# Kernel optimization log

Measured on AMD Instinct MI355X. Metric: run time of the kernel, lower is better.

## Reference

```python
import jax, jax.numpy as jnp
import numpy as np

N, M = 30000, 16
NFEAT, NCLASS = 1024, 16
K, DD = 8, 32          # ncaps, nhidden (delta_d)
D = K * DD             # rep_dim = 256
NLAYER = 3


def _l2norm(x, axis):
    n = jnp.linalg.norm(x, axis=axis, keepdims=True)
    return x / jnp.maximum(n, 1e-12)


def _routing(x, neighbors, max_iter, param, fc_w=None, fc_b=None):
    # x: [n, d]; neighbors: [n, m] int indices in [0, n] (n = zero pad row)
    n = x.shape[0]
    m = neighbors.shape[1]
    if fc_w is not None:  # first layer: per-capsule linear + relu
        x_dis = _l2norm(x.reshape(n, K, DD), axis=2)
        # torch Linear: y = x @ W.T + b, per capsule k
        x = jax.nn.relu(jnp.einsum('nki,koi->nko', x_dis, fc_w) + fc_b)
        x = x.reshape(n, D)
    x = _l2norm(x.reshape(n, K, DD), axis=2).reshape(n, D)
    z_tab = jnp.concatenate([x, jnp.zeros((1, D), x.dtype)], axis=0)
    z = z_tab[neighbors].reshape(n, m, K, DD)  # [n,m,k,dd] neighbor gather
    u_before = x.reshape(n, K, DD)
    u = None
    p1 = None
    for it in range(max_iter):
        if u is None:
            p = jnp.zeros((n, m, K), x.dtype)
        else:
            p = jnp.einsum('nmkd,nkd->nmk', z, u)
        p1 = jax.nn.softmax(p, axis=1)  # over neighbors
        u1 = jnp.einsum('nmkd,nmk->nkd', z, p1)
        p2 = jax.nn.softmax(p, axis=2)  # over capsules
        u2 = jnp.einsum('nmkd,nmk->nkd', z, p2)
        u = param * u1 + (1.0 - param) * u2 + u_before
        u_before = u
        if it < max_iter - 1:
            u = _l2norm(u, axis=2)
    return u.reshape(n, D), p1


def setup_inputs() -> dict:
    key = jax.random.key(0)
    ks = jax.random.split(key, 8)
    s = 1.0 / np.sqrt(D)
    return {
        'x': jax.random.normal(ks[0], (N, NFEAT), jnp.float32),
        'neighbors': jax.random.randint(ks[1], (N, M), 0, N).astype(jnp.int32),
        'pca_w': jax.random.normal(ks[2], (NFEAT, D), jnp.float32) * s,
        'pca_b': jax.random.normal(ks[3], (D,), jnp.float32) * s,
        'raw_param': jnp.ones((1,), jnp.float32),
        'fc_w': jax.random.normal(ks[4], (K, DD, DD), jnp.float32) * (1.0 / np.sqrt(DD)),
        'fc_b': jax.random.normal(ks[5], (K, DD), jnp.float32) * 0.01,
        'mlp_w': jax.random.normal(ks[6], (NCLASS, D), jnp.float32) * s,
        'mlp_b': jax.random.normal(ks[7], (NCLASS,), jnp.float32) * s,
        'routit': 6,
    }


def reference(x, neighbors, pca_w, pca_b, raw_param, fc_w, fc_b, mlp_w, mlp_b, routit):
    # pca projection (eval mode: dropout is identity)
    h = jax.nn.relu(x @ pca_w + pca_b)
    param = jax.nn.sigmoid(raw_param[0])
    for i in range(NLAYER - 1):
        h, _ = _routing(h, neighbors, routit, param,
                        fc_w if i == 0 else None, fc_b if i == 0 else None)
        h = jax.nn.relu(h)
    h, _ = _routing(h, neighbors, routit, param,
                    fc_w if NLAYER == 1 else None, fc_b if NLAYER == 1 else None)
    logit = h @ mlp_w.T + mlp_b
    log_probs = jax.nn.log_softmax(logit, axis=1)
    return log_probs, h  # (classifier output, embedding)
```

## Files before the change

### kernel.cpp

```cpp
#include <hip/hip_runtime.h>

#define NN 30000
#define MMN 16
#define NF 1024
#define NC 16
#define KC 8
#define DDIM 32
#define DR 256

typedef __bf16 bf16x8 __attribute__((ext_vector_type(8)));
typedef __bf16 bf16x4 __attribute__((ext_vector_type(4)));
typedef float floatx4 __attribute__((ext_vector_type(4)));

__device__ inline void splitbf(float v, __bf16& h, __bf16& l) {
  h = (__bf16)v;
  l = (__bf16)(v - (float)h);
}

template <int C>
__device__ __forceinline__ float dppadd(float x) {
  return x + __int_as_float(
      __builtin_amdgcn_update_dpp(0, __float_as_int(x), C, 0xF, 0xF, true));
}
template <int C>
__device__ __forceinline__ float dppmov(float x) {
  return __int_as_float(
      __builtin_amdgcn_update_dpp(0, __float_as_int(x), C, 0xF, 0xF, true));
}
__device__ __forceinline__ float red8(float x) {
  x = dppadd<0xB1>(x);
  x = dppadd<0x4E>(x);
  x = dppadd<0x141>(x);
  return x;
}
__device__ __forceinline__ float redk(float x) {
  x = dppadd<0x128>(x);
  x = x + __int_as_float(__builtin_amdgcn_ds_swizzle(__float_as_int(x), 0x401F));
  x = x + __shfl_xor(x, 32);
  return x;
}
__device__ __forceinline__ float red16sum(float x) {
  x = dppadd<0xB1>(x);
  x = dppadd<0x4E>(x);
  x = x + __int_as_float(__builtin_amdgcn_ds_swizzle(__float_as_int(x), 0x101F));
  x = x + __int_as_float(__builtin_amdgcn_ds_swizzle(__float_as_int(x), 0x201F));
  return x;
}
__device__ __forceinline__ float red16max(float x) {
  x = fmaxf(x, dppmov<0xB1>(x));
  x = fmaxf(x, dppmov<0x4E>(x));
  x = fmaxf(x, __int_as_float(__builtin_amdgcn_ds_swizzle(__float_as_int(x), 0x101F)));
  x = fmaxf(x, __int_as_float(__builtin_amdgcn_ds_swizzle(__float_as_int(x), 0x201F)));
  return x;
}

__device__ __forceinline__ float rscatter8(const float p[8], int lane) {
  const bool j4 = (lane & 4) != 0, j2 = (lane & 2) != 0, j1 = (lane & 1) != 0;
  float k0 = j4 ? p[4] : p[0];
  float k1 = j4 ? p[5] : p[1];
  float k2 = j4 ? p[6] : p[2];
  float k3 = j4 ? p[7] : p[3];
  float s0 = j4 ? p[0] : p[4];
  float s1 = j4 ? p[1] : p[5];
  float s2 = j4 ? p[2] : p[6];
  float s3 = j4 ? p[3] : p[7];
  k0 += dppmov<0x141>(s0); k1 += dppmov<0x141>(s1);
  k2 += dppmov<0x141>(s2); k3 += dppmov<0x141>(s3);
  float t0 = j2 ? k2 : k0;
  float t1 = j2 ? k3 : k1;
  float u0 = j2 ? k0 : k2;
  float u1 = j2 ? k1 : k3;
  t0 += dppmov<0x4E>(u0); t1 += dppmov<0x4E>(u1);
  float a = j1 ? t1 : t0;
  float b = j1 ? t0 : t1;
  a += dppmov<0xB1>(b);
  return a;
}

__device__ __forceinline__ void agather8(float a, float w[8], int lane) {
  const bool j4 = (lane & 4) != 0, j2 = (lane & 2) != 0, j1 = (lane & 1) != 0;
  float pa = dppmov<0xB1>(a);
  float b0 = j1 ? pa : a;
  float b1 = j1 ? a : pa;
  float p0 = dppmov<0x4E>(b0), p1 = dppmov<0x4E>(b1);
  float q0 = j2 ? p0 : b0;
  float q1 = j2 ? p1 : b1;
  float q2 = j2 ? b0 : p0;
  float q3 = j2 ? b1 : p1;
  float m0 = dppmov<0x141>(q0), m1 = dppmov<0x141>(q1);
  float m2 = dppmov<0x141>(q2), m3 = dppmov<0x141>(q3);
  w[0] = j4 ? m0 : q0;  w[1] = j4 ? m1 : q1;
  w[2] = j4 ? m2 : q2;  w[3] = j4 ? m3 : q3;
  w[4] = j4 ? q0 : m0;  w[5] = j4 ? q1 : m1;
  w[6] = j4 ? q2 : m2;  w[7] = j4 ? q3 : m3;
}

__global__ __launch_bounds__(256) void wt_build_kernel(
    const float* __restrict__ w, __bf16* __restrict__ wt_hi, __bf16* __restrict__ wt_lo) {
  const int gid  = blockIdx.x * 256 + threadIdx.x;
  const int lane = gid & 63;
  const int kc   = gid >> 10;
  const int g    = (gid >> 6) & 15;
  const int c = g * 16 + (lane & 15);
  const int k = kc * 32 + (lane >> 4) * 8;
  bf16x8 h, l;
#pragma unroll
  for (int j = 0; j < 8; ++j) {
    const float v = w[(size_t)(k + j) * DR + c];
    __bf16 hh, ll; splitbf(v, hh, ll);
    h[j] = hh; l[j] = ll;
  }
  *(bf16x8*)(wt_hi + (size_t)gid * 8) = h;
  *(bf16x8*)(wt_lo + (size_t)gid * 8) = l;
}

__global__ void pad_zero_kernel(float* __restrict__ p) {
  ((float4*)p)[threadIdx.x] = make_float4(0.f, 0.f, 0.f, 0.f);
}

__global__ __launch_bounds__(256, 4) void pca_mfma_kernel(
    const float* __restrict__ x, const __bf16* __restrict__ wt_hi,
    const __bf16* __restrict__ wt_lo, const float* __restrict__ b,
    float* __restrict__ out) {
  __shared__ __bf16 Ah[128][40];
  __shared__ __bf16 Al[128][40];
  const int t    = threadIdx.x;
  const int lane = t & 63;
  const int wv   = t >> 6;
  const int q    = lane >> 4;
  const int lm   = lane & 15;
  const int rowBase = (blockIdx.x >> 2) << 7;
  const int cg      = (blockIdx.x & 3) << 2;
  const int colBase = cg << 4;

  const int sr = t >> 2;
  const int sc = (t & 3) << 2;

  floatx4 acc[2][4];
#pragma unroll
  for (int rt = 0; rt < 2; ++rt)
#pragma unroll
    for (int ct = 0; ct < 4; ++ct)
      acc[rt][ct] = (floatx4){0.f, 0.f, 0.f, 0.f};

  const float* xrA = x + (size_t)(rowBase + sr) * NF + sc;
  const float* xrB = x + (size_t)(rowBase + sr + 64) * NF + sc;
  const bool okA = (rowBase + sr) < NN;
  const bool okB = (rowBase + sr + 64) < NN;

  const __bf16* wfh = wt_hi + ((size_t)cg << 9) + (lane << 3);
  const __bf16* wfl = wt_lo + ((size_t)cg << 9) + (lane << 3);

  float4 xv[4];
  xv[0] = okA ? *(const float4*)(xrA)      : make_float4(0.f, 0.f, 0.f, 0.f);
  xv[1] = okA ? *(const float4*)(xrA + 16) : make_float4(0.f, 0.f, 0.f, 0.f);
  xv[2] = okB ? *(const float4*)(xrB)      : make_float4(0.f, 0.f, 0.f, 0.f);
  xv[3] = okB ? *(const float4*)(xrB + 16) : make_float4(0.f, 0.f, 0.f, 0.f);

  for (int k0 = 0; k0 < NF; k0 += 32) {
    const int kc = k0 >> 5;
    bf16x8 bh[4], bl[4];
#pragma unroll
    for (int ct = 0; ct < 4; ++ct) {
      bh[ct] = *(const bf16x8*)(wfh + (((size_t)kc << 4) + ct) * 512);
      bl[ct] = *(const bf16x8*)(wfl + (((size_t)kc << 4) + ct) * 512);
    }
    asm volatile("s_waitcnt lgkmcnt(0)" ::: "memory");
    __builtin_amdgcn_s_barrier();
    {
#pragma unroll
      for (int i = 0; i < 4; ++i) {
        bf16x4 h4, l4;
        const float vs[4] = {xv[i].x, xv[i].y, xv[i].z, xv[i].w};
#pragma unroll
        for (int j = 0; j < 4; ++j) { __bf16 H, L; splitbf(vs[j], H, L); h4[j] = H; l4[j] = L; }
        const int row = sr + (i >> 1) * 64;
        const int col = sc + (i & 1) * 16;
        *(bf16x4*)&Ah[row][col] = h4;
        *(bf16x4*)&Al[row][col] = l4;
      }
    }
    float4 xn[4];
    if (k0 + 32 < NF) {
      xn[0] = okA ? *(const float4*)(xrA + k0 + 32) : make_float4(0.f, 0.f, 0.f, 0.f);
      xn[1] = okA ? *(const float4*)(xrA + k0 + 48) : make_float4(0.f, 0.f, 0.f, 0.f);
      xn[2] = okB ? *(const float4*)(xrB + k0 + 32) : make_float4(0.f, 0.f, 0.f, 0.f);
      xn[3] = okB ? *(const float4*)(xrB + k0 + 48) : make_float4(0.f, 0.f, 0.f, 0.f);
    } else {
#pragma unroll
      for (int i = 0; i < 4; ++i) xn[i] = make_float4(0.f, 0.f, 0.f, 0.f);
    }
    asm volatile("s_waitcnt lgkmcnt(0)" ::: "memory");
    __builtin_amdgcn_s_barrier();
#pragma unroll
    for (int rt = 0; rt < 2; ++rt) {
      const int ar = (wv << 5) + (rt << 4) + lm;
      const bf16x8 ah = *(const bf16x8*)&Ah[ar][q << 3];
      const bf16x8 al = *(const bf16x8*)&Al[ar][q << 3];
#pragma unroll
      for (int ct = 0; ct < 4; ++ct) {
        acc[rt][ct] = __builtin_amdgcn_mfma_f32_16x16x32_bf16(ah, bh[ct], acc[rt][ct], 0, 0, 0);
        acc[rt][ct] = __builtin_amdgcn_mfma_f32_16x16x32_bf16(ah, bl[ct], acc[rt][ct], 0, 0, 0);
        acc[rt][ct] = __builtin_amdgcn_mfma_f32_16x16x32_bf16(al, bh[ct], acc[rt][ct], 0, 0, 0);
      }
    }
#pragma unroll
    for (int i = 0; i < 4; ++i) xv[i] = xn[i];
  }
#pragma unroll
  for (int rt = 0; rt < 2; ++rt) {
#pragma unroll
    for (int ct = 0; ct < 4; ++ct) {
      const int col = colBase + (ct << 4) + lm;
      const float bias = b[col];
#pragma unroll
      for (int r = 0; r < 4; ++r) {
        const int row = rowBase + (wv << 5) + (rt << 4) + (q << 2) + r;
        if (row < NN) out[(size_t)row * DR + col] = fmaxf(acc[rt][ct][r] + bias, 0.f);
      }
    }
  }
}

__global__ __launch_bounds__(256, 4) void norm_fc_kernel(
    const float* __restrict__ hin, const float* __restrict__ fcw,
    const float* __restrict__ fcb, float* __restrict__ q) {
  const int k = blockIdx.y;
  const int n = blockIdx.x * 256 + threadIdx.x;
  if (n > NN) return;
  float* qrow = q + (size_t)n * DR + k * DDIM;
  if (n == NN) {
#pragma unroll
    for (int i = 0; i < DDIM; i += 4)
      *(float4*)(qrow + i) = make_float4(0.f, 0.f, 0.f, 0.f);
    return;
  }
  const float* hrow = hin + (size_t)n * DR + k * DDIM;
  float v[DDIM];
  float ss = 0.f;
#pragma unroll
  for (int i = 0; i < DDIM; i += 4) {
    float4 tv = *(const float4*)(hrow + i);
    tv.x = fmaxf(tv.x, 0.f); tv.y = fmaxf(tv.y, 0.f);
    tv.z = fmaxf(tv.z, 0.f); tv.w = fmaxf(tv.w, 0.f);
    v[i] = tv.x; v[i+1] = tv.y; v[i+2] = tv.z; v[i+3] = tv.w;
    ss += tv.x*tv.x + tv.y*tv.y + tv.z*tv.z + tv.w*tv.w;
  }
  float inv = 1.f / fmaxf(sqrtf(ss), 1e-12f);
#pragma unroll
  for (int i = 0; i < DDIM; ++i) v[i] *= inv;
#pragma unroll
  for (int i = 0; i < DDIM; ++i) asm volatile("" : "+v"(v[i]));
  float y[DDIM];
  ss = 0.f;
  const float* wk = fcw + (size_t)k * DDIM * DDIM;
  const float* bk = fcb + k * DDIM;
#pragma unroll 4
  for (int o = 0; o < DDIM; ++o) {
    float a = bk[o];
#pragma unroll
    for (int i = 0; i < DDIM; i += 4) {
      const float4 wv = *(const float4*)(wk + o * DDIM + i);
      a += v[i]*wv.x + v[i+1]*wv.y + v[i+2]*wv.z + v[i+3]*wv.w;
    }
    a = fmaxf(a, 0.f);
    y[o] = a;
    ss += a * a;
  }
  inv = 1.f / fmaxf(sqrtf(ss), 1e-12f);
#pragma unroll
  for (int o = 0; o < DDIM; o += 4) {
    float4 tv;
    tv.x = y[o]*inv; tv.y = y[o+1]*inv; tv.z = y[o+2]*inv; tv.w = y[o+3]*inv;
    *(float4*)(qrow + o) = tv;
  }
}

__global__ __launch_bounds__(256, 4) void routing_kernel(
    const float* __restrict__ tab, const float* __restrict__ padrow,
    const int* __restrict__ nbr, const float* __restrict__ rawp,
    const int* __restrict__ ritp, float* __restrict__ uout, const int doNorm) {
  const int lane = threadIdx.x & 63;
  const int node = blockIdx.x * 4 + (threadIdx.x >> 6);
  const int off = (lane >> 3) * DDIM + (lane & 7) * 4;
  const float param = 1.f / (1.f + __expf(-rawp[0]));
  const float qparam = 1.f - param;
  const int iters = ritp[0];

  float4 z[MMN];
#pragma unroll
  for (int m = 0; m < MMN; ++m) {
    const int j = nbr[node * MMN + m];
    const float* zrow = (j == NN) ? padrow : (tab + (size_t)j * DR);
    z[m] = *(const float4*)(zrow + off);
  }
  float4 ub = *(const float4*)(tab + (size_t)node * DR + off);

  float4 S = make_float4(0.f, 0.f, 0.f, 0.f);
#pragma unroll
  for (int m = 0; m < MMN; ++m) {
    S.x += z[m].x; S.y += z[m].y; S.z += z[m].z; S.w += z[m].w;
  }
  const float w0 = param * 0.0625f + qparam * 0.125f;
  ub.x += w0 * S.x; ub.y += w0 * S.y; ub.z += w0 * S.z; ub.w += w0 * S.w;

  float4 u = ub;
  if (iters > 1) {
    float ss = red8(ub.x*ub.x + ub.y*ub.y + ub.z*ub.z + ub.w*ub.w);
    const float inv = 1.f / fmaxf(sqrtf(ss), 1e-12f);
    u.x = ub.x*inv; u.y = ub.y*inv; u.z = ub.z*inv; u.w = ub.w*inv;
  }

  for (int it = 1; it < iters; ++it) {
    float pA[8], pB[8];
#pragma unroll
    for (int m = 0; m < 8; ++m) {
      pA[m] = z[m].x*u.x + z[m].y*u.y + z[m].z*u.z + z[m].w*u.w;
      pB[m] = z[m+8].x*u.x + z[m+8].y*u.y + z[m+8].z*u.z + z[m+8].w*u.w;
    }
    const float dA = rscatter8(pA, lane);
    const float dB = rscatter8(pB, lane);
    const float eA = __expf(dA);
    const float eB = __expf(dB);
    const float smk = red8(eA + eB);
    const float skA = redk(eA);
    const float skB = redk(eB);
    const float c1 = param * __builtin_amdgcn_rcpf(smk);
    const float wA = eA * (c1 + qparam * __builtin_amdgcn_rcpf(skA));
    const float wB = eB * (c1 + qparam * __builtin_amdgcn_rcpf(skB));
    float wS[8], wT[8];
    agather8(wA, wS, lane);
    agather8(wB, wT, lane);
    float4 un = ub;
#pragma unroll
    for (int m = 0; m < 8; ++m) {
      un.x += wS[m]*z[m].x;   un.y += wS[m]*z[m].y;
      un.z += wS[m]*z[m].z;   un.w += wS[m]*z[m].w;
      un.x += wT[m]*z[m+8].x; un.y += wT[m]*z[m+8].y;
      un.z += wT[m]*z[m+8].z; un.w += wT[m]*z[m+8].w;
    }
    ub = un;
    if (it < iters - 1) {
      float ss = red8(un.x*un.x + un.y*un.y + un.z*un.z + un.w*un.w);
      const float inv = 1.f / fmaxf(sqrtf(ss), 1e-12f);
      u.x = un.x*inv; u.y = un.y*inv; u.z = un.z*inv; u.w = un.w*inv;
    }
  }
  float4 w = ub;
  if (doNorm) {
    w.x = fmaxf(w.x, 0.f); w.y = fmaxf(w.y, 0.f);
    w.z = fmaxf(w.z, 0.f); w.w = fmaxf(w.w, 0.f);
    float ss = red8(w.x*w.x + w.y*w.y + w.z*w.z + w.w*w.w);
    const float inv = 1.f / fmaxf(sqrtf(ss), 1e-12f);
    w.x *= inv; w.y *= inv; w.z *= inv; w.w *= inv;
  }
  *(float4*)(uout + (size_t)node * DR + off) = w;
}

__global__ __launch_bounds__(256) void mlp_kernel(
    const float* __restrict__ h, const float* __restrict__ w,
    const float* __restrict__ b, float* __restrict__ out) {
  const int lane = threadIdx.x & 63;
  const int wv   = threadIdx.x >> 6;
  const int q    = lane >> 4;
  const int lm   = lane & 15;
  const int nodeTile = blockIdx.x * 64 + wv * 16;
  const int nodeA = nodeTile + lm;
  const bool okA = nodeA < NN;
  const float* hp = h + (size_t)nodeA * DR + (q << 3);
  const float* wp = w + (size_t)lm * DR + (q << 3);

  floatx4 acc = (floatx4){0.f, 0.f, 0.f, 0.f};
#pragma unroll
  for (int kc = 0; kc < 8; ++kc) {
    bf16x8 ah, al, bh, bl;
    {
      float va[8];
      if (okA) {
        *(float4*)&va[0] = *(const float4*)(hp + kc * 32);
        *(float4*)&va[4] = *(const float4*)(hp + kc * 32 + 4);
      } else {
#pragma unroll
        for (int j = 0; j < 8; ++j) va[j] = 0.f;
      }
#pragma unroll
      for (int j = 0; j < 8; ++j) { __bf16 H, L; splitbf(va[j], H, L); ah[j] = H; al[j] = L; }
    }
    {
      float vb[8];
      *(float4*)&vb[0] = *(const float4*)(wp + kc * 32);
      *(float4*)&vb[4] = *(const float4*)(wp + kc * 32 + 4);
#pragma unroll
      for (int j = 0; j < 8; ++j) { __bf16 H, L; splitbf(vb[j], H, L); bh[j] = H; bl[j] = L; }
    }
    acc = __builtin_amdgcn_mfma_f32_16x16x32_bf16(ah, bh, acc, 0, 0, 0);
    acc = __builtin_amdgcn_mfma_f32_16x16x32_bf16(ah, bl, acc, 0, 0, 0);
    acc = __builtin_amdgcn_mfma_f32_16x16x32_bf16(al, bh, acc, 0, 0, 0);
  }
  const float bias = b[lm];
#pragma unroll
  for (int r = 0; r < 4; ++r) {
    const int nrow = nodeTile + (q << 2) + r;
    const float lg = acc[r] + bias;
    const float mx = red16max(lg);
    const float e  = __expf(lg - mx);
    const float se = red16sum(e);
    const float lp = lg - mx - __logf(se);
    if (nrow < NN) out[(size_t)nrow * NC + lm] = lp;
  }
}

extern "C" void kernel_launch(void* const* d_in, const int* in_sizes, int n_in,
                              void* d_out, int out_size, void* d_ws, size_t ws_size,
                              hipStream_t stream) {
  const float* x     = (const float*)d_in[0];
  const int*   nbr   = (const int*)  d_in[1];
  const float* pca_w = (const float*)d_in[2];
  const float* pca_b = (const float*)d_in[3];
  const float* rawp  = (const float*)d_in[4];
  const float* fc_w  = (const float*)d_in[5];
  const float* fc_b  = (const float*)d_in[6];
  const float* mlp_w = (const float*)d_in[7];
  const float* mlp_b = (const float*)d_in[8];
  const int*   ritp  = (const int*)  d_in[9];

  float* out  = (float*)d_out;
  float* EMB  = out + (size_t)NN * NC;
  float* Bpad = EMB - DR;
  float* Q    = (float*)d_ws;
  float* Qpad = Q + (size_t)NN * DR;

  __bf16* wt_hi = (__bf16*)d_out;
  __bf16* wt_lo = wt_hi + (size_t)DR * NF;

  wt_build_kernel<<<128, 256, 0, stream>>>(pca_w, wt_hi, wt_lo);
  pad_zero_kernel<<<1, 64, 0, stream>>>(Bpad);
  pca_mfma_kernel<<<((NN + 127) / 128) * 4, 256, 0, stream>>>(x, wt_hi, wt_lo, pca_b, EMB);
  norm_fc_kernel<<<dim3((NN + 1 + 255) / 256, KC), 256, 0, stream>>>(EMB, fc_w, fc_b, Q);
  routing_kernel<<<NN / 4, 256, 0, stream>>>(Q, Qpad, nbr, rawp, ritp, EMB, 1);
  routing_kernel<<<NN / 4, 256, 0, stream>>>(EMB, Bpad, nbr, rawp, ritp, Q, 1);
  routing_kernel<<<NN / 4, 256, 0, stream>>>(Q, Qpad, nbr, rawp, ritp, EMB, 0);
  mlp_kernel<<<(NN + 63) / 64, 256, 0, stream>>>(EMB, mlp_w, mlp_b, out);
}
```

Measured before the change: 530.2 us.

## Retile PCA GEMM so each block covers all 256 columns over 64 rows

```diff
diff --git a/kernel.cpp b/kernel.cpp
--- a/kernel.cpp
+++ b/kernel.cpp
@@ -118,106 +118,85 @@
   ((float4*)p)[threadIdx.x] = make_float4(0.f, 0.f, 0.f, 0.f);
 }
 
-__global__ __launch_bounds__(256, 4) void pca_mfma_kernel(
+__global__ __launch_bounds__(256, 2) void pca_mfma_kernel(
     const float* __restrict__ x, const __bf16* __restrict__ wt_hi,
     const __bf16* __restrict__ wt_lo, const float* __restrict__ b,
     float* __restrict__ out) {
-  __shared__ __bf16 Ah[128][40];
-  __shared__ __bf16 Al[128][40];
+  __shared__ __bf16 Ah[64][40];
+  __shared__ __bf16 Al[64][40];
   const int t    = threadIdx.x;
   const int lane = t & 63;
   const int wv   = t >> 6;
   const int q    = lane >> 4;
   const int lm   = lane & 15;
-  const int rowBase = (blockIdx.x >> 2) << 7;
-  const int cg      = (blockIdx.x & 3) << 2;
-  const int colBase = cg << 4;
+  const int rowBase = blockIdx.x << 6;
 
   const int sr = t >> 2;
-  const int sc = (t & 3) << 2;
-
-  floatx4 acc[2][4];
-#pragma unroll
-  for (int rt = 0; rt < 2; ++rt)
-#pragma unroll
-    for (int ct = 0; ct < 4; ++ct)
-      acc[rt][ct] = (floatx4){0.f, 0.f, 0.f, 0.f};
-
-  const float* xrA = x + (size_t)(rowBase + sr) * NF + sc;
-  const float* xrB = x + (size_t)(rowBase + sr + 64) * NF + sc;
-  const bool okA = (rowBase + sr) < NN;
-  const bool okB = (rowBase + sr + 64) < NN;
-
-  const __bf16* wfh = wt_hi + ((size_t)cg << 9) + (lane << 3);
-  const __bf16* wfl = wt_lo + ((size_t)cg << 9) + (lane << 3);
-
-  float4 xv[4];
-  xv[0] = okA ? *(const float4*)(xrA)      : make_float4(0.f, 0.f, 0.f, 0.f);
-  xv[1] = okA ? *(const float4*)(xrA + 16) : make_float4(0.f, 0.f, 0.f, 0.f);
-  xv[2] = okB ? *(const float4*)(xrB)      : make_float4(0.f, 0.f, 0.f, 0.f);
-  xv[3] = okB ? *(const float4*)(xrB + 16) : make_float4(0.f, 0.f, 0.f, 0.f);
+  const int sc = (t & 3) << 3;
+
+  floatx4 acc[16];
+#pragma unroll
+  for (int ct = 0; ct < 16; ++ct) acc[ct] = (floatx4){0.f, 0.f, 0.f, 0.f};
+
+  const float* xr = x + (size_t)(rowBase + sr) * NF + sc;
+  const bool ok = (rowBase + sr) < NN;
+
+  const __bf16* wfh = wt_hi + (lane << 3);
+  const __bf16* wfl = wt_lo + (lane << 3);
+
+  float4 xv[2];
+  xv[0] = ok ? *(const float4*)(xr)     : make_float4(0.f, 0.f, 0.f, 0.f);
+  xv[1] = ok ? *(const float4*)(xr + 4) : make_float4(0.f, 0.f, 0.f, 0.f);
 
   for (int k0 = 0; k0 < NF; k0 += 32) {
     const int kc = k0 >> 5;
-    bf16x8 bh[4], bl[4];
-#pragma unroll
-    for (int ct = 0; ct < 4; ++ct) {
-      bh[ct] = *(const bf16x8*)(wfh + (((size_t)kc << 4) + ct) * 512);
-      bl[ct] = *(const bf16x8*)(wfl + (((size_t)kc << 4) + ct) * 512);
-    }
     asm volatile("s_waitcnt lgkmcnt(0)" ::: "memory");
     __builtin_amdgcn_s_barrier();
     {
-#pragma unroll
-      for (int i = 0; i < 4; ++i) {
-        bf16x4 h4, l4;
-        const float vs[4] = {xv[i].x, xv[i].y, xv[i].z, xv[i].w};
-#pragma unroll
-        for (int j = 0; j < 4; ++j) { __bf16 H, L; splitbf(vs[j], H, L); h4[j] = H; l4[j] = L; }
-        const int row = sr + (i >> 1) * 64;
-        const int col = sc + (i & 1) * 16;
-        *(bf16x4*)&Ah[row][col] = h4;
-        *(bf16x4*)&Al[row][col] = l4;
-      }
-    }
-    float4 xn[4];
-    if (k0 + 32 < NF) {
-      xn[0] = okA ? *(const float4*)(xrA + k0 + 32) : make_float4(0.f, 0.f, 0.f, 0.f);
-      xn[1] = okA ? *(const float4*)(xrA + k0 + 48) : make_float4(0.f, 0.f, 0.f, 0.f);
-      xn[2] = okB ? *(const float4*)(xrB + k0 + 32) : make_float4(0.f, 0.f, 0.f, 0.f);
-      xn[3] = okB ? *(const float4*)(xrB + k0 + 48) : make_float4(0.f, 0.f, 0.f, 0.f);
+      bf16x8 h8, l8;
+      const float vs[8] = {xv[0].x, xv[0].y, xv[0].z, xv[0].w,
+                           xv[1].x, xv[1].y, xv[1].z, xv[1].w};
+#pragma unroll
+      for (int j = 0; j < 8; ++j) { __bf16 H, L; splitbf(vs[j], H, L); h8[j] = H; l8[j] = L; }
+      *(bf16x8*)&Ah[sr][sc] = h8;
+      *(bf16x8*)&Al[sr][sc] = l8;
+    }
+    float4 xn[2];
+    if (k0 + 32 < NF && ok) {
+      xn[0] = *(const float4*)(xr + k0 + 32);
+      xn[1] = *(const float4*)(xr + k0 + 36);
     } else {
-#pragma unroll
-      for (int i = 0; i < 4; ++i) xn[i] = make_float4(0.f, 0.f, 0.f, 0.f);
+      xn[0] = make_float4(0.f, 0.f, 0.f, 0.f);
+      xn[1] = make_float4(0.f, 0.f, 0.f, 0.f);
     }
     asm volatile("s_waitcnt lgkmcnt(0)" ::: "memory");
     __builtin_amdgcn_s_barrier();
-#pragma unroll
-    for (int rt = 0; rt < 2; ++rt) {
-      const int ar = (wv << 5) + (rt << 4) + lm;
-      const bf16x8 ah = *(const bf16x8*)&Ah[ar][q << 3];
-      const bf16x8 al = *(const bf16x8*)&Al[ar][q << 3];
-#pragma unroll
-      for (int ct = 0; ct < 4; ++ct) {
-        acc[rt][ct] = __builtin_amdgcn_mfma_f32_16x16x32_bf16(ah, bh[ct], acc[rt][ct], 0, 0, 0);
-        acc[rt][ct] = __builtin_amdgcn_mfma_f32_16x16x32_bf16(ah, bl[ct], acc[rt][ct], 0, 0, 0);
-        acc[rt][ct] = __builtin_amdgcn_mfma_f32_16x16x32_bf16(al, bh[ct], acc[rt][ct], 0, 0, 0);
+    const int ar = (wv << 4) + lm;
+    const bf16x8 ah = *(const bf16x8*)&Ah[ar][q << 3];
+    const bf16x8 al = *(const bf16x8*)&Al[ar][q << 3];
+#pragma unroll
+    for (int g = 0; g < 4; ++g) {
+#pragma unroll
+      for (int j = 0; j < 4; ++j) {
+        const int ct = g * 4 + j;
+        const bf16x8 bh = *(const bf16x8*)(wfh + (((size_t)kc << 4) + ct) * 512);
+        const bf16x8 bl = *(const bf16x8*)(wfl + (((size_t)kc << 4) + ct) * 512);
+        acc[ct] = __builtin_amdgcn_mfma_f32_16x16x32_bf16(ah, bh, acc[ct], 0, 0, 0);
+        acc[ct] = __builtin_amdgcn_mfma_f32_16x16x32_bf16(ah, bl, acc[ct], 0, 0, 0);
+        acc[ct] = __builtin_amdgcn_mfma_f32_16x16x32_bf16(al, bh, acc[ct], 0, 0, 0);
       }
     }
-#pragma unroll
-    for (int i = 0; i < 4; ++i) xv[i] = xn[i];
-  }
-#pragma unroll
-  for (int rt = 0; rt < 2; ++rt) {
-#pragma unroll
-    for (int ct = 0; ct < 4; ++ct) {
-      const int col = colBase + (ct << 4) + lm;
-      const float bias = b[col];
-#pragma unroll
-      for (int r = 0; r < 4; ++r) {
-        const int row = rowBase + (wv << 5) + (rt << 4) + (q << 2) + r;
-        if (row < NN) out[(size_t)row * DR + col] = fmaxf(acc[rt][ct][r] + bias, 0.f);
-      }
+    xv[0] = xn[0];
+    xv[1] = xn[1];
+  }
+#pragma unroll
+  for (int ct = 0; ct < 16; ++ct) {
+    const int col = (ct << 4) + lm;
+    const float bias = b[col];
+#pragma unroll
+    for (int r = 0; r < 4; ++r) {
+      const int row = rowBase + (wv << 4) + (q << 2) + r;
+      if (row < NN) out[(size_t)row * DR + col] = fmaxf(acc[ct][r] + bias, 0.f);
     }
   }
 }
@@ -435,7 +414,7 @@
 
   wt_build_kernel<<<128, 256, 0, stream>>>(pca_w, wt_hi, wt_lo);
   pad_zero_kernel<<<1, 64, 0, stream>>>(Bpad);
-  pca_mfma_kernel<<<((NN + 127) / 128) * 4, 256, 0, stream>>>(x, wt_hi, wt_lo, pca_b, EMB);
+  pca_mfma_kernel<<<(NN + 63) / 64, 256, 0, stream>>>(x, wt_hi, wt_lo, pca_b, EMB);
   norm_fc_kernel<<<dim3((NN + 1 + 255) / 256, KC), 256, 0, stream>>>(EMB, fc_w, fc_b, Q);
   routing_kernel<<<NN / 4, 256, 0, stream>>>(Q, Qpad, nbr, rawp, ritp, EMB, 1);
   routing_kernel<<<NN / 4, 256, 0, stream>>>(EMB, Bpad, nbr, rawp, ritp, Q, 1);
```

Result: slower. 612.4 us (+15.5%).
